# Kernel tuning notes

Measured on AMD Instinct MI355X. Metric: run time of the kernel, lower is better.

The kernel has to match this reference:

```python
import jax, jax.numpy as jnp
import numpy as np

B, N, D = 8, 4096, 512
H, DH = 8, 64
W = 128            # window_size
DISP = W // 2      # cyclic shift displacement
NEG = -1e9         # stands in for float('-inf') in the additive mask


def setup_inputs() -> dict:
    key = jax.random.key(0)
    ks = jax.random.split(key, 5)
    return {
        "x": jax.random.normal(ks[0], (B, N, D), dtype=jnp.float32),
        "Wqkv": jax.random.normal(ks[1], (D, 3 * H * DH), dtype=jnp.float32) * (1.0 / np.sqrt(D)),
        "pos_emb": jax.random.normal(ks[2], (2 * W - 1,), dtype=jnp.float32),
        "Wout": jax.random.normal(ks[3], (H * DH, D), dtype=jnp.float32) * (1.0 / np.sqrt(H * DH)),
        "bout": jax.random.normal(ks[4], (D,), dtype=jnp.float32),
    }


def _shift_mask(w, disp, dtype):
    # create_mask(..., MASK=True): -inf wherever query and key fall on
    # opposite sides of the displacement boundary.
    i = jnp.arange(w)
    cross = (i[:, None] >= w - disp) != (i[None, :] >= w - disp)
    return jnp.where(cross, jnp.asarray(NEG, dtype), jnp.asarray(0.0, dtype))


def reference(x, Wqkv, pos_emb, Wout, bout):
    b, n, d = x.shape
    p = n // W  # new_p: number of windows
    scale = DH ** -0.5

    # cyclic shift
    xs = jnp.roll(x, -DISP, axis=1)

    qkv = xs @ Wqkv  # [b, n, 3*H*DH]
    q, k, v = jnp.split(qkv, 3, axis=-1)

    # rearrange 'b (new_w new_p) (head dim) -> b head new_p new_w dim'
    # window index is the OUTER factor of the token dim (strided windows).
    def win(t):
        return t.reshape(b, W, p, H, DH).transpose(0, 3, 2, 1, 4)  # [b,h,p,w,dh]

    q, k, v = win(q), win(k), win(v)

    dots = jnp.einsum('bhpid,bhpjd->bhpij', q, k) * scale  # [b,h,p,w,w]

    # relative position bias: 1D distance table
    rel_idx = jnp.arange(W)[None, :] - jnp.arange(W)[:, None] + (W - 1)  # [w,w]
    dots = dots + pos_emb[rel_idx]

    # shift mask: torch code adds it to dots[:, :, -p:], i.e. every window
    dots = dots + _shift_mask(W, DISP, dots.dtype)

    attn = jax.nn.softmax(dots, axis=-1)
    out = jnp.einsum('bhpij,bhpjd->bhpid', attn, v)  # [b,h,p,w,dh]

    # rearrange 'b head patch window dim -> b (patch window) (head dim)'
    out = out.transpose(0, 2, 3, 1, 4).reshape(b, n, H * DH)
    out = out @ Wout + bout

    # cyclic back shift
    return jnp.roll(out, DISP, axis=1)
```

## Files before the change

### kernel.cpp

```cpp
#include <hip/hip_runtime.h>
#include <hip/hip_bf16.h>

#define BB   8
#define NN   4096
#define DD   512
#define HH   8
#define DHH  64
#define WW   128
#define PP   32
#define DISP 64

typedef __attribute__((ext_vector_type(8))) short bf16x8_t;
typedef __attribute__((ext_vector_type(4))) float f32x4_t;
typedef __attribute__((ext_vector_type(8))) unsigned short u16x8;

__device__ __forceinline__ unsigned short f2bf(float f) {
    unsigned int u = __float_as_uint(f);
    unsigned int r = (u + 0x7FFFu + ((u >> 16) & 1u)) >> 16;
    return (unsigned short)r;
}
__device__ __forceinline__ float bf2f(unsigned short u) {
    return __uint_as_float(((unsigned int)u) << 16);
}

__device__ __forceinline__ void gload_lds16(const void* g, void* l) {
    __builtin_amdgcn_global_load_lds(
        (const __attribute__((address_space(1))) unsigned int*)g,
        (__attribute__((address_space(3))) unsigned int*)l, 16, 0, 0);
}

__global__ __launch_bounds__(256) void cvt_x_shift(const float* __restrict__ x,
                                                   unsigned short* __restrict__ xb) {
    int idx = blockIdx.x * 256 + threadIdx.x;
    int e0 = idx * 8;
    int r = e0 >> 9, d = e0 & 511;
    int b = r >> 12, n = r & 4095;
    const float* src = x + (size_t)((b << 12) | ((n + DISP) & 4095)) * 512 + d;
    float4 f0 = *(const float4*)src;
    float4 f1 = *(const float4*)(src + 4);
    u16x8 p;
    p[0] = f2bf(f0.x); p[1] = f2bf(f0.y); p[2] = f2bf(f0.z); p[3] = f2bf(f0.w);
    p[4] = f2bf(f1.x); p[5] = f2bf(f1.y); p[6] = f2bf(f1.z); p[7] = f2bf(f1.w);
    *(u16x8*)(xb + (size_t)r * 512 + d) = p;
}

__global__ __launch_bounds__(256) void cvt_w(const float* __restrict__ Wqkv,
                                             const float* __restrict__ Wout,
                                             unsigned short* __restrict__ wqkvT,
                                             unsigned short* __restrict__ woutT) {
    int idx = blockIdx.x * 256 + threadIdx.x;
    if (idx < 786432) {
        int n = idx >> 9, k = idx & 511;
        wqkvT[idx] = f2bf(Wqkv[(size_t)k * 1536 + n]);
    } else {
        int j = idx - 786432;
        int n = j >> 9, k = j & 511;
        woutT[j] = f2bf(Wout[(size_t)k * 512 + n]);
    }
}

__global__ __launch_bounds__(256) void gemm_qkv(const unsigned short* __restrict__ A,
                                                const unsigned short* __restrict__ BT,
                                                unsigned short* __restrict__ qw,
                                                unsigned short* __restrict__ kw,
                                                unsigned short* __restrict__ vw) {
    __shared__ unsigned short As[128 * 32];
    __shared__ unsigned short Bs[128 * 32];
    const int tid  = threadIdx.x;
    const int wv   = tid >> 6, lane = tid & 63;
    const int brow = blockIdx.x;
    const int bcol = blockIdx.y;
    const int b  = brow >> 5, pi = brow & 31;
    const int wr = (wv >> 1) * 64, wc = (wv & 1) * 64;
    const int lr = lane >> 4, lc = lane & 15;
    const int kq = lr * 8;

    f32x4_t acc[4][4];
#pragma unroll
    for (int i = 0; i < 4; ++i)
#pragma unroll
        for (int j = 0; j < 4; ++j) acc[i][j] = (f32x4_t)0.f;

    const size_t abase = ((size_t)b * 4096 + pi) * 512;
    const size_t brow0 = (size_t)bcol * 128;

    for (int k0 = 0; k0 < 512; k0 += 32) {
#pragma unroll
        for (int i = 0; i < 2; ++i) {
            int chunk = wv * 2 + i;
            int idx = chunk * 64 + lane;
            int row = idx >> 2;
            int koff = (idx & 3) * 8;
            gload_lds16(A  + abase + (size_t)row * 16384 + k0 + koff, &As[chunk * 512]);
            gload_lds16(BT + (brow0 + row) * 512 + k0 + koff, &Bs[chunk * 512]);
        }
        __syncthreads();
        bf16x8_t af[4], bfr[4];
#pragma unroll
        for (int mi = 0; mi < 4; ++mi)
            af[mi] = *(const bf16x8_t*)&As[(wr + mi * 16 + lc) * 32 + kq];
#pragma unroll
        for (int nj = 0; nj < 4; ++nj)
            bfr[nj] = *(const bf16x8_t*)&Bs[(wc + nj * 16 + lc) * 32 + kq];
#pragma unroll
        for (int mi = 0; mi < 4; ++mi)
#pragma unroll
            for (int nj = 0; nj < 4; ++nj)
                acc[mi][nj] = __builtin_amdgcn_mfma_f32_16x16x32_bf16(
                    af[mi], bfr[nj], acc[mi][nj], 0, 0, 0);
        __syncthreads();
    }

#pragma unroll
    for (int nj = 0; nj < 4; ++nj) {
        int c = bcol * 128 + wc + nj * 16 + lc;
        int which = c >> 9;
        int h  = (c >> 6) & 7;
        int dh = c & 63;
        unsigned short* dst = (which == 0) ? qw : ((which == 1) ? kw : vw);
        size_t base = ((size_t)((b * 8 + h) * 32 + pi)) * 8192;
#pragma unroll
        for (int mi = 0; mi < 4; ++mi)
#pragma unroll
            for (int r = 0; r < 4; ++r) {
                int w = wr + mi * 16 + lr * 4 + r;
                size_t off;
                if (which == 0)      off = base + (size_t)w * 64 + dh;
                else if (which == 1) off = base + (size_t)w * 64 + (dh ^ ((w & 7) << 3));
                else                 off = base + (size_t)dh * 128 + (w ^ ((dh & 7) << 3));
                dst[off] = f2bf(acc[mi][nj][r]);
            }
    }
}

__global__ __launch_bounds__(256) void gemm_out(const unsigned short* __restrict__ A,
                                                const unsigned short* __restrict__ BT,
                                                const float* __restrict__ bout,
                                                float* __restrict__ out) {
    __shared__ unsigned short As[128 * 32];
    __shared__ unsigned short Bs[128 * 32];
    const int tid  = threadIdx.x;
    const int wv   = tid >> 6, lane = tid & 63;
    const int brow = blockIdx.x;
    const int bcol = blockIdx.y;
    const int wr = (wv >> 1) * 64, wc = (wv & 1) * 64;
    const int lr = lane >> 4, lc = lane & 15;
    const int kq = lr * 8;

    f32x4_t acc[4][4];
#pragma unroll
    for (int i = 0; i < 4; ++i)
#pragma unroll
        for (int j = 0; j < 4; ++j) acc[i][j] = (f32x4_t)0.f;

    const size_t arow0 = (size_t)brow * 128;
    const size_t brow0 = (size_t)bcol * 128;

    for (int k0 = 0; k0 < 512; k0 += 32) {
#pragma unroll
        for (int i = 0; i < 2; ++i) {
            int chunk = wv * 2 + i;
            int idx = chunk * 64 + lane;
            int row = idx >> 2;
            int koff = (idx & 3) * 8;
            gload_lds16(A  + (arow0 + row) * 512 + k0 + koff, &As[chunk * 512]);
            gload_lds16(BT + (brow0 + row) * 512 + k0 + koff, &Bs[chunk * 512]);
        }
        __syncthreads();
        bf16x8_t af[4], bfr[4];
#pragma unroll
        for (int mi = 0; mi < 4; ++mi)
            af[mi] = *(const bf16x8_t*)&As[(wr + mi * 16 + lc) * 32 + kq];
#pragma unroll
        for (int nj = 0; nj < 4; ++nj)
            bfr[nj] = *(const bf16x8_t*)&Bs[(wc + nj * 16 + lc) * 32 + kq];
#pragma unroll
        for (int mi = 0; mi < 4; ++mi)
#pragma unroll
            for (int nj = 0; nj < 4; ++nj)
                acc[mi][nj] = __builtin_amdgcn_mfma_f32_16x16x32_bf16(
                    af[mi], bfr[nj], acc[mi][nj], 0, 0, 0);
        __syncthreads();
    }

#pragma unroll
    for (int nj = 0; nj < 4; ++nj) {
        int c = bcol * 128 + wc + nj * 16 + lc;
        float bias = bout[c];
#pragma unroll
        for (int mi = 0; mi < 4; ++mi)
#pragma unroll
            for (int r = 0; r < 4; ++r) {
                int row = brow * 128 + wr + mi * 16 + lr * 4 + r;
                int b = row >> 12, np = row & 4095;
                int dn = (np + DISP) & 4095;
                out[(size_t)((b << 12) | dn) * 512 + c] = acc[mi][nj][r] + bias;
            }
    }
}

__global__ __launch_bounds__(256) void win_attn(const unsigned short* __restrict__ qw,
                                                const unsigned short* __restrict__ kw,
                                                const unsigned short* __restrict__ vw,
                                                const float* __restrict__ pos,
                                                unsigned short* __restrict__ aob) {
    __shared__ unsigned short K_lds[8192];
    __shared__ unsigned short V_lds[8192];
    __shared__ unsigned short P_lds[4][4096];
    __shared__ float pos_lds[255];

    const int tid  = threadIdx.x;
    const int wv   = tid >> 6, lane = tid & 63;
    const int lr   = lane >> 4, lc = lane & 15;
    const int blk  = blockIdx.x;
    const int pi   = blk & 31;
    const int h    = (blk >> 5) & 7;
    const int b    = blk >> 8;
    const size_t base = ((size_t)((b * 8 + h) * 32 + pi)) * 8192;
    const unsigned short* qg = qw + base;
    const unsigned short* kg = kw + base;
    const unsigned short* vg = vw + base;

    if (tid < 255) pos_lds[tid] = pos[tid];

#pragma unroll
    for (int i = 0; i < 4; ++i) {
        int c = wv * 4 + i;
        gload_lds16(kg + c * 512 + lane * 8, &K_lds[c * 512]);
        gload_lds16(vg + c * 512 + lane * 8, &V_lds[c * 512]);
    }

    bf16x8_t qf[2][2];
#pragma unroll
    for (int mi = 0; mi < 2; ++mi)
#pragma unroll
        for (int ks = 0; ks < 2; ++ks)
            qf[mi][ks] = *(const bf16x8_t*)(qg + (wv * 32 + mi * 16 + lc) * 64 + ks * 32 + lr * 8);

    __syncthreads();

    f32x4_t sa[2][8];
#pragma unroll
    for (int mi = 0; mi < 2; ++mi)
#pragma unroll
        for (int nj = 0; nj < 8; ++nj) sa[mi][nj] = (f32x4_t)0.f;

#pragma unroll
    for (int ks = 0; ks < 2; ++ks) {
#pragma unroll
        for (int nj = 0; nj < 8; ++nj) {
            int row = nj * 16 + lc;
            int byteoff = ((row * 128) + (ks * 32 + lr * 8) * 2) ^ ((row & 7) << 4);
            bf16x8_t kf = *(const bf16x8_t*)((const char*)K_lds + byteoff);
            sa[0][nj] = __builtin_amdgcn_mfma_f32_16x16x32_bf16(qf[0][ks], kf, sa[0][nj], 0, 0, 0);
            sa[1][nj] = __builtin_amdgcn_mfma_f32_16x16x32_bf16(qf[1][ks], kf, sa[1][nj], 0, 0, 0);
        }
    }

#pragma unroll
    for (int mi = 0; mi < 2; ++mi)
#pragma unroll
        for (int r = 0; r < 4; ++r) {
            int i = wv * 32 + mi * 16 + lr * 4 + r;
            float mx = -3.0e38f;
#pragma unroll
            for (int nj = 0; nj < 8; ++nj) {
                int j = nj * 16 + lc;
                float s = fmaf(sa[mi][nj][r], 0.125f, pos_lds[j - i + 127]);
                if ((i >= 64) != (j >= 64)) s -= 1e9f;
                sa[mi][nj][r] = s;
                mx = fmaxf(mx, s);
            }
            mx = fmaxf(mx, __shfl_xor(mx, 1));
            mx = fmaxf(mx, __shfl_xor(mx, 2));
            mx = fmaxf(mx, __shfl_xor(mx, 4));
            mx = fmaxf(mx, __shfl_xor(mx, 8));
            float sum = 0.f;
#pragma unroll
            for (int nj = 0; nj < 8; ++nj) {
                float e = __expf(sa[mi][nj][r] - mx);
                sa[mi][nj][r] = e;
                sum += e;
            }
            sum += __shfl_xor(sum, 1);
            sum += __shfl_xor(sum, 2);
            sum += __shfl_xor(sum, 4);
            sum += __shfl_xor(sum, 8);
            float inv = 1.0f / sum;
            int rloc = mi * 16 + lr * 4 + r;
#pragma unroll
            for (int nj = 0; nj < 8; ++nj) {
                int j = nj * 16 + lc;
                int byteoff = ((rloc * 256) + j * 2) ^ ((rloc & 7) << 4);
                *(unsigned short*)((char*)P_lds[wv] + byteoff) = f2bf(sa[mi][nj][r] * inv);
            }
        }

    f32x4_t oa[2][4];
#pragma unroll
    for (int mi = 0; mi < 2; ++mi)
#pragma unroll
        for (int nj = 0; nj < 4; ++nj) oa[mi][nj] = (f32x4_t)0.f;

#pragma unroll
    for (int ks = 0; ks < 4; ++ks) {
        bf16x8_t pa[2], vb[4];
#pragma unroll
        for (int mi = 0; mi < 2; ++mi) {
            int rloc = mi * 16 + lc;
            int byteoff = ((rloc * 256) + (ks * 32 + lr * 8) * 2) ^ ((rloc & 7) << 4);
            pa[mi] = *(const bf16x8_t*)((const char*)P_lds[wv] + byteoff);
        }
#pragma unroll
        for (int nj = 0; nj < 4; ++nj) {
            int dh = nj * 16 + lc;
            int byteoff = ((dh * 256) + (ks * 32 + lr * 8) * 2) ^ ((dh & 7) << 4);
            vb[nj] = *(const bf16x8_t*)((const char*)V_lds + byteoff);
        }
#pragma unroll
        for (int mi = 0; mi < 2; ++mi)
#pragma unroll
            for (int nj = 0; nj < 4; ++nj)
                oa[mi][nj] = __builtin_amdgcn_mfma_f32_16x16x32_bf16(pa[mi], vb[nj], oa[mi][nj], 0, 0, 0);
    }

    const size_t orow0 = (size_t)b * 4096 + (size_t)pi * 128;
#pragma unroll
    for (int mi = 0; mi < 2; ++mi)
#pragma unroll
        for (int r = 0; r < 4; ++r) {
            int w = wv * 32 + mi * 16 + lr * 4 + r;
            unsigned short* dst = aob + (orow0 + w) * 512 + h * 64;
#pragma unroll
            for (int nj = 0; nj < 4; ++nj)
                dst[nj * 16 + lc] = f2bf(oa[mi][nj][r]);
        }
}

extern "C" void kernel_launch(void* const* d_in, const int* in_sizes, int n_in,
                              void* d_out, int out_size, void* d_ws, size_t ws_size,
                              hipStream_t stream) {
    (void)in_sizes; (void)n_in; (void)out_size; (void)ws_size;
    const float* x    = (const float*)d_in[0];
    const float* Wqkv = (const float*)d_in[1];
    const float* pos  = (const float*)d_in[2];
    const float* Wout = (const float*)d_in[3];
    const float* bout = (const float*)d_in[4];
    float* out = (float*)d_out;

    const size_t T = (size_t)BB * NN * 512;
    unsigned short* xb    = (unsigned short*)d_ws;
    unsigned short* wqkvT = xb + T;
    unsigned short* woutT = wqkvT + 786432;
    unsigned short* qw    = woutT + 262144;
    unsigned short* kw    = qw + T;
    unsigned short* vw    = kw + T;
    unsigned short* aob   = vw + T;

    cvt_x_shift<<<dim3(8192), 256, 0, stream>>>(x, xb);
    cvt_w<<<dim3(4096), 256, 0, stream>>>(Wqkv, Wout, wqkvT, woutT);
    gemm_qkv<<<dim3(256, 12), 256, 0, stream>>>(xb, wqkvT, qw, kw, vw);
    win_attn<<<dim3(2048), 256, 0, stream>>>(qw, kw, vw, pos, aob);
    gemm_out<<<dim3(256, 4), 256, 0, stream>>>(aob, woutT, bout, out);
}
```

Baseline: 307.9 us.

## Double-buffer LDS tiles in QKV and output projection GEMMs

```diff
diff --git a/kernel.cpp b/kernel.cpp
--- a/kernel.cpp
+++ b/kernel.cpp
@@ -64,8 +64,8 @@
                                                 unsigned short* __restrict__ qw,
                                                 unsigned short* __restrict__ kw,
                                                 unsigned short* __restrict__ vw) {
-    __shared__ unsigned short As[128 * 32];
-    __shared__ unsigned short Bs[128 * 32];
+    __shared__ unsigned short As[2][128 * 32];
+    __shared__ unsigned short Bs[2][128 * 32];
     const int tid  = threadIdx.x;
     const int wv   = tid >> 6, lane = tid & 63;
     const int brow = blockIdx.x;
@@ -84,32 +84,52 @@
     const size_t abase = ((size_t)b * 4096 + pi) * 512;
     const size_t brow0 = (size_t)bcol * 128;
 
-    for (int k0 = 0; k0 < 512; k0 += 32) {
-#pragma unroll
-        for (int i = 0; i < 2; ++i) {
-            int chunk = wv * 2 + i;
-            int idx = chunk * 64 + lane;
-            int row = idx >> 2;
-            int koff = (idx & 3) * 8;
-            gload_lds16(A  + abase + (size_t)row * 16384 + k0 + koff, &As[chunk * 512]);
-            gload_lds16(BT + (brow0 + row) * 512 + k0 + koff, &Bs[chunk * 512]);
-        }
+#define STAGE_Q(BUF, K0S) do {                                                   \
+    _Pragma("unroll")                                                            \
+    for (int i_ = 0; i_ < 2; ++i_) {                                             \
+        int chunk_ = wv * 2 + i_;                                                \
+        int idx_ = chunk_ * 64 + lane;                                           \
+        int row_ = idx_ >> 2;                                                    \
+        int koff_ = (idx_ & 3) * 8;                                              \
+        gload_lds16(A  + abase + (size_t)row_ * 16384 + (K0S) + koff_,           \
+                    &As[BUF][chunk_ * 512]);                                     \
+        gload_lds16(BT + (brow0 + row_) * 512 + (K0S) + koff_,                   \
+                    &Bs[BUF][chunk_ * 512]);                                     \
+    } } while (0)
+
+#define COMPUTE_Q(BUF) do {                                                      \
+    bf16x8_t af_[4], bf_[4];                                                     \
+    _Pragma("unroll")                                                            \
+    for (int mi_ = 0; mi_ < 4; ++mi_)                                            \
+        af_[mi_] = *(const bf16x8_t*)&As[BUF][(wr + mi_ * 16 + lc) * 32 + kq];   \
+    _Pragma("unroll")                                                            \
+    for (int nj_ = 0; nj_ < 4; ++nj_)                                            \
+        bf_[nj_] = *(const bf16x8_t*)&Bs[BUF][(wc + nj_ * 16 + lc) * 32 + kq];   \
+    _Pragma("unroll")                                                            \
+    for (int mi_ = 0; mi_ < 4; ++mi_)                                            \
+        _Pragma("unroll")                                                        \
+        for (int nj_ = 0; nj_ < 4; ++nj_)                                        \
+            acc[mi_][nj_] = __builtin_amdgcn_mfma_f32_16x16x32_bf16(             \
+                af_[mi_], bf_[nj_], acc[mi_][nj_], 0, 0, 0);                     \
+    } while (0)
+
+    STAGE_Q(0, 0);
+    __syncthreads();
+#pragma unroll 1
+    for (int t = 0; t < 7; ++t) {
+        STAGE_Q(1, (2 * t + 1) * 32);
+        COMPUTE_Q(0);
         __syncthreads();
-        bf16x8_t af[4], bfr[4];
-#pragma unroll
-        for (int mi = 0; mi < 4; ++mi)
-            af[mi] = *(const bf16x8_t*)&As[(wr + mi * 16 + lc) * 32 + kq];
-#pragma unroll
-        for (int nj = 0; nj < 4; ++nj)
-            bfr[nj] = *(const bf16x8_t*)&Bs[(wc + nj * 16 + lc) * 32 + kq];
-#pragma unroll
-        for (int mi = 0; mi < 4; ++mi)
-#pragma unroll
-            for (int nj = 0; nj < 4; ++nj)
-                acc[mi][nj] = __builtin_amdgcn_mfma_f32_16x16x32_bf16(
-                    af[mi], bfr[nj], acc[mi][nj], 0, 0, 0);
+        STAGE_Q(0, (2 * t + 2) * 32);
+        COMPUTE_Q(1);
         __syncthreads();
     }
+    STAGE_Q(1, 15 * 32);
+    COMPUTE_Q(0);
+    __syncthreads();
+    COMPUTE_Q(1);
+#undef STAGE_Q
+#undef COMPUTE_Q
 
 #pragma unroll
     for (int nj = 0; nj < 4; ++nj) {
@@ -137,8 +157,8 @@
                                                 const unsigned short* __restrict__ BT,
                                                 const float* __restrict__ bout,
                                                 float* __restrict__ out) {
-    __shared__ unsigned short As[128 * 32];
-    __shared__ unsigned short Bs[128 * 32];
+    __shared__ unsigned short As[2][128 * 32];
+    __shared__ unsigned short Bs[2][128 * 32];
     const int tid  = threadIdx.x;
     const int wv   = tid >> 6, lane = tid & 63;
     const int brow = blockIdx.x;
@@ -156,32 +176,52 @@
     const size_t arow0 = (size_t)brow * 128;
     const size_t brow0 = (size_t)bcol * 128;
 
-    for (int k0 = 0; k0 < 512; k0 += 32) {
-#pragma unroll
-        for (int i = 0; i < 2; ++i) {
-            int chunk = wv * 2 + i;
-            int idx = chunk * 64 + lane;
-            int row = idx >> 2;
-            int koff = (idx & 3) * 8;
-            gload_lds16(A  + (arow0 + row) * 512 + k0 + koff, &As[chunk * 512]);
-            gload_lds16(BT + (brow0 + row) * 512 + k0 + koff, &Bs[chunk * 512]);
-        }
+#define STAGE_O(BUF, K0S) do {                                                   \
+    _Pragma("unroll")                                                            \
+    for (int i_ = 0; i_ < 2; ++i_) {                                             \
+        int chunk_ = wv * 2 + i_;                                                \
+        int idx_ = chunk_ * 64 + lane;                                           \
+        int row_ = idx_ >> 2;                                                    \
+        int koff_ = (idx_ & 3) * 8;                                              \
+        gload_lds16(A  + (arow0 + row_) * 512 + (K0S) + koff_,                   \
+                    &As[BUF][chunk_ * 512]);                                     \
+        gload_lds16(BT + (brow0 + row_) * 512 + (K0S) + koff_,                   \
+                    &Bs[BUF][chunk_ * 512]);                                     \
+    } } while (0)
+
+#define COMPUTE_O(BUF) do {                                                      \
+    bf16x8_t af_[4], bf_[4];                                                     \
+    _Pragma("unroll")                                                            \
+    for (int mi_ = 0; mi_ < 4; ++mi_)                                            \
+        af_[mi_] = *(const bf16x8_t*)&As[BUF][(wr + mi_ * 16 + lc) * 32 + kq];   \
+    _Pragma("unroll")                                                            \
+    for (int nj_ = 0; nj_ < 4; ++nj_)                                            \
+        bf_[nj_] = *(const bf16x8_t*)&Bs[BUF][(wc + nj_ * 16 + lc) * 32 + kq];   \
+    _Pragma("unroll")                                                            \
+    for (int mi_ = 0; mi_ < 4; ++mi_)                                            \
+        _Pragma("unroll")                                                        \
+        for (int nj_ = 0; nj_ < 4; ++nj_)                                        \
+            acc[mi_][nj_] = __builtin_amdgcn_mfma_f32_16x16x32_bf16(             \
+                af_[mi_], bf_[nj_], acc[mi_][nj_], 0, 0, 0);                     \
+    } while (0)
+
+    STAGE_O(0, 0);
+    __syncthreads();
+#pragma unroll 1
+    for (int t = 0; t < 7; ++t) {
+        STAGE_O(1, (2 * t + 1) * 32);
+        COMPUTE_O(0);
         __syncthreads();
-        bf16x8_t af[4], bfr[4];
-#pragma unroll
-        for (int mi = 0; mi < 4; ++mi)
-            af[mi] = *(const bf16x8_t*)&As[(wr + mi * 16 + lc) * 32 + kq];
-#pragma unroll
-        for (int nj = 0; nj < 4; ++nj)
-            bfr[nj] = *(const bf16x8_t*)&Bs[(wc + nj * 16 + lc) * 32 + kq];
-#pragma unroll
-        for (int mi = 0; mi < 4; ++mi)
-#pragma unroll
-            for (int nj = 0; nj < 4; ++nj)
-                acc[mi][nj] = __builtin_amdgcn_mfma_f32_16x16x32_bf16(
-                    af[mi], bfr[nj], acc[mi][nj], 0, 0, 0);
+        STAGE_O(0, (2 * t + 2) * 32);
+        COMPUTE_O(1);
         __syncthreads();
     }
+    STAGE_O(1, 15 * 32);
+    COMPUTE_O(0);
+    __syncthreads();
+    COMPUTE_O(1);
+#undef STAGE_O
+#undef COMPUTE_O
 
 #pragma unroll
     for (int nj = 0; nj < 4; ++nj) {
```

Measured after the change: 311.5 us. About the same (+1.2%).
